# Kernel tuning notes

Hardware: AMD Instinct MI355X
Metric: run time of the kernel (lower is better)

The kernel has to match this reference:

```python
import jax, jax.numpy as jnp
import numpy as np
import math

B, T, D_IN, D_OUT = 4, 2048, 2048, 2048

def _inv_sigmoid(v):
    return math.log(v / (1 - v + 1e-08))

def setup_inputs() -> dict:
    key = jax.random.key(0)
    ks = jax.random.split(key, 6)
    x = jax.random.normal(ks[0], (B, T, D_IN), dtype=jnp.float32)
    W_p = jax.random.normal(ks[1], (D_OUT, D_IN), dtype=jnp.float32) * 0.02
    W_i = jax.random.normal(ks[2], (D_OUT, D_IN), dtype=jnp.float32) * 0.002
    W_d = jax.random.normal(ks[3], (D_OUT, D_IN), dtype=jnp.float32) * 0.002
    alpha_logit = jnp.full((D_IN,), _inv_sigmoid(0.9), dtype=jnp.float32)
    beta_logit = jnp.full((D_IN,), _inv_sigmoid(0.5), dtype=jnp.float32)
    W_gate_w = jax.random.normal(ks[4], (3, 3 * D_IN), dtype=jnp.float32) * 0.01
    W_gate_b = jnp.array([1.0, 0.0, 0.0], dtype=jnp.float32)
    bias = jnp.zeros((D_OUT,), dtype=jnp.float32)
    return {"x": x, "W_p": W_p, "W_i": W_i, "W_d": W_d,
            "alpha_logit": alpha_logit, "beta_logit": beta_logit,
            "W_gate_w": W_gate_w, "W_gate_b": W_gate_b, "bias": bias}

def _pid_features(x, alpha, beta):
    # x: (B,T,D). Single scan computing EMA integral and smoothed derivative.
    x_t = jnp.swapaxes(x, 0, 1)  # (T,B,D)
    x_prev = jnp.concatenate([jnp.zeros_like(x_t[:1]), x_t[:-1]], axis=0)
    diff_t = x_t - x_prev  # raw finite difference
    def step(carry, inp):
        s, d = carry
        xt, dt = inp
        s = alpha * s + (1.0 - alpha) * xt
        d = beta * d + (1.0 - beta) * dt
        return (s, d), (s, d)
    s0 = jnp.zeros(x.shape[::2], dtype=x.dtype)  # (B,D)
    _, (integ_t, deriv_t) = jax.lax.scan(step, (s0, s0), (x_t, diff_t))
    return jnp.swapaxes(integ_t, 0, 1), jnp.swapaxes(deriv_t, 0, 1)

def reference(x, W_p, W_i, W_d, alpha_logit, beta_logit, W_gate_w, W_gate_b, bias):
    alpha = jax.nn.sigmoid(alpha_logit)  # (D,)
    beta = jax.nn.sigmoid(beta_logit)
    integral, derivative = _pid_features(x, alpha, beta)  # (B,T,D) each
    gate_in = jnp.concatenate([x, integral, derivative], axis=-1)  # (B,T,3D)
    logits = jnp.einsum('btk,gk->btg', gate_in, W_gate_w) + W_gate_b
    gates = jax.nn.softmax(logits, axis=-1)  # (B,T,3)
    p_out = jnp.einsum('btd,od->bto', x, W_p)
    i_out = jnp.einsum('btd,od->bto', integral, W_i)
    d_out = jnp.einsum('btd,od->bto', derivative, W_d)
    y = gates[..., 0:1] * p_out + gates[..., 1:2] * i_out + gates[..., 2:3] * d_out + bias
    return y
```

## Files before the change

### kernel.cpp

```cpp
#include <hip/hip_runtime.h>
#include <stdint.h>

typedef unsigned short u16;

#define GAS __attribute__((address_space(1)))
#define LAS __attribute__((address_space(3)))

typedef __bf16 bf16x8 __attribute__((ext_vector_type(8)));
typedef float f32x4 __attribute__((ext_vector_type(4)));


__device__ inline u16 f2b(float f) {
    uint32_t x = __float_as_uint(f);
    uint32_t r = (x + 0x7fffu + ((x >> 16) & 1u)) >> 16;
    return (u16)r;
}

__device__ inline float b2f(u16 u) {
    union { uint32_t i; float f; } v;
    v.i = ((uint32_t)u) << 16;
    return v.f;
}

__device__ inline void load8b(float* v, const u16* p) {
    uint4 u = *(const uint4*)p;
    v[0] = b2f((u16)(u.x)); v[1] = b2f((u16)(u.x >> 16));
    v[2] = b2f((u16)(u.y)); v[3] = b2f((u16)(u.y >> 16));
    v[4] = b2f((u16)(u.z)); v[5] = b2f((u16)(u.z >> 16));
    v[6] = b2f((u16)(u.w)); v[7] = b2f((u16)(u.w >> 16));
}

__device__ inline void load8f(float* v, const float* p) {
    float4 a = *(const float4*)p;
    float4 b = *(const float4*)(p + 4);
    v[0] = a.x; v[1] = a.y; v[2] = a.z; v[3] = a.w;
    v[4] = b.x; v[5] = b.y; v[6] = b.z; v[7] = b.w;
}

__device__ inline void store8b(u16* p, const float* v, float scale) {
    uint4 u;
    u.x = (uint32_t)f2b(v[0] * scale) | ((uint32_t)f2b(v[1] * scale) << 16);
    u.y = (uint32_t)f2b(v[2] * scale) | ((uint32_t)f2b(v[3] * scale) << 16);
    u.z = (uint32_t)f2b(v[4] * scale) | ((uint32_t)f2b(v[5] * scale) << 16);
    u.w = (uint32_t)f2b(v[6] * scale) | ((uint32_t)f2b(v[7] * scale) << 16);
    *(uint4*)p = u;
}

__device__ inline float sigmoidf(float v) { return 1.f / (1.f + __expf(-v)); }

__device__ inline float pow64f(float a) {
    float p = a * a;
    p = p * p;
    p = p * p;
    p = p * p;
    p = p * p;
    return p * p;
}

__device__ inline float* carry_ptr(u16* Z, int plane, int b, int c, int d) {
    int f = ((plane * 4 + b) * 32 + c) * 2048 + d;
    int row = f >> 10;
    int off = f & 1023;
    return (float*)(Z + (size_t)row * 6144) + off;
}

__global__ __launch_bounds__(256) void pack_w(
    const float* __restrict__ Wp, const float* __restrict__ Wi,
    const float* __restrict__ Wd, u16* __restrict__ Wcat)
{
    int i = (blockIdx.x * 256 + threadIdx.x) * 8;
    int seg = i >> 22;
    int j = i & 4194303;
    const float* src = (seg == 0) ? Wp : (seg == 1) ? Wi : Wd;
    int o = j >> 11;
    int c = j & 2047;
    float v[8];
    load8f(v, src + j);
    store8b(Wcat + (size_t)o * 6144 + seg * 2048 + c, v, 1.0f);
}

__global__ __launch_bounds__(256) void scan_pass1(
    const float* __restrict__ x, const float* __restrict__ alog,
    const float* __restrict__ blog, u16* __restrict__ Z)
{
    const int d = blockIdx.x * 256 + threadIdx.x;
    const int c = blockIdx.y;
    const int b = blockIdx.z;
    const float alpha = sigmoidf(alog[d]);
    const float beta  = sigmoidf(blog[d]);
    const float oma = 1.f - alpha, omb = 1.f - beta;
    const float* xp = x + ((size_t)b * 2048 + c * 64) * 2048 + d;
    float xprev = (c == 0) ? 0.f : xp[-2048];
    float s = 0.f, dd = 0.f;
    #pragma unroll 8
    for (int t = 0; t < 64; ++t) {
        float xf = xp[(size_t)t * 2048];
        s = alpha * s + oma * xf;
        dd = beta * dd + omb * (xf - xprev);
        xprev = xf;
    }
    *carry_ptr(Z, 0, b, c, d) = s;
    *carry_ptr(Z, 1, b, c, d) = dd;
}

__global__ __launch_bounds__(256) void scan_pass2(
    const float* __restrict__ alog, const float* __restrict__ blog,
    u16* __restrict__ Z)
{
    const int g = blockIdx.x * 256 + threadIdx.x;
    const int b = g >> 11;
    const int d = g & 2047;
    const float aL = pow64f(sigmoidf(alog[d]));
    const float bL = pow64f(sigmoidf(blog[d]));
    float sIn = 0.f, dIn = 0.f;
    for (int c = 0; c < 32; ++c) {
        float* sp = carry_ptr(Z, 0, b, c, d);
        float* dp = carry_ptr(Z, 1, b, c, d);
        float sl = *sp, dl = *dp;
        *sp = sIn; *dp = dIn;
        sIn = sl + aL * sIn;
        dIn = dl + bL * dIn;
    }
}

__global__ __launch_bounds__(256) void scan_pass3(
    const float* __restrict__ x, const float* __restrict__ alog,
    const float* __restrict__ blog, u16* __restrict__ Z)
{
    const int d = blockIdx.x * 256 + threadIdx.x;
    const int c = blockIdx.y;
    const int b = blockIdx.z;
    const float alpha = sigmoidf(alog[d]);
    const float beta  = sigmoidf(blog[d]);
    const float oma = 1.f - alpha, omb = 1.f - beta;
    const float* xp = x + ((size_t)b * 2048 + c * 64) * 2048 + d;
    u16* zp = Z + ((size_t)b * 2048 + c * 64) * 6144 + 2048 + d;
    float s  = *carry_ptr(Z, 0, b, c, d);
    float dd = *carry_ptr(Z, 1, b, c, d);
    float xprev = (c == 0) ? 0.f : xp[-2048];
    #pragma unroll 8
    for (int t = 0; t < 64; ++t) {
        float xf = xp[(size_t)t * 2048];
        s = alpha * s + oma * xf;
        dd = beta * dd + omb * (xf - xprev);
        xprev = xf;
        size_t zo = (size_t)t * 6144;
        zp[zo] = f2b(s);
        zp[zo + 2048] = f2b(dd);
    }
}

__global__ __launch_bounds__(256) void gates_kernel(
    const float* __restrict__ x, const float* __restrict__ Wg,
    const float* __restrict__ Wgb, u16* __restrict__ Z)
{
    const int row = blockIdx.x;
    const int tid = threadIdx.x;
    const int k = tid * 8;
    const float* xr = x + (size_t)row * 2048;
    u16* zr = Z + (size_t)row * 6144;

    float xv[8], sv[8], dv[8];
    load8f(xv, xr + k);
    load8b(sv, zr + 2048 + k);
    load8b(dv, zr + 4096 + k);

    float p[3];
    #pragma unroll
    for (int gg = 0; gg < 3; ++gg) {
        float wx[8], ws[8], wd[8];
        load8f(wx, Wg + gg * 6144 + k);
        load8f(ws, Wg + gg * 6144 + 2048 + k);
        load8f(wd, Wg + gg * 6144 + 4096 + k);
        float acc = 0.f;
        #pragma unroll
        for (int j = 0; j < 8; ++j)
            acc += xv[j] * wx[j] + sv[j] * ws[j] + dv[j] * wd[j];
        p[gg] = acc;
    }

    #pragma unroll
    for (int off = 32; off > 0; off >>= 1) {
        p[0] += __shfl_down(p[0], off);
        p[1] += __shfl_down(p[1], off);
        p[2] += __shfl_down(p[2], off);
    }

    __shared__ float red[4][3];
    __shared__ float gsh[3];
    int wv = tid >> 6, lane = tid & 63;
    if (lane == 0) { red[wv][0] = p[0]; red[wv][1] = p[1]; red[wv][2] = p[2]; }
    __syncthreads();
    if (tid == 0) {
        float l0 = red[0][0] + red[1][0] + red[2][0] + red[3][0] + Wgb[0];
        float l1 = red[0][1] + red[1][1] + red[2][1] + red[3][1] + Wgb[1];
        float l2 = red[0][2] + red[1][2] + red[2][2] + red[3][2] + Wgb[2];
        float m = fmaxf(l0, fmaxf(l1, l2));
        float e0 = __expf(l0 - m), e1 = __expf(l1 - m), e2 = __expf(l2 - m);
        float inv = 1.f / (e0 + e1 + e2);
        gsh[0] = e0 * inv; gsh[1] = e1 * inv; gsh[2] = e2 * inv;
    }
    __syncthreads();
    float g0 = gsh[0], g1 = gsh[1], g2 = gsh[2];
    store8b(zr + k, xv, g0);
    store8b(zr + 2048 + k, sv, g1);
    store8b(zr + 4096 + k, dv, g2);
}

__global__ __launch_bounds__(256, 3) void gemm_kernel(
    const u16* __restrict__ Z, const u16* __restrict__ Wcat,
    const float* __restrict__ bias, float* __restrict__ out)
{
    __shared__ u16 a_sh[128 * 64];
    __shared__ u16 b_sh[128 * 64];

    const int tid = threadIdx.x;
    const int bm = blockIdx.y * 128;
    const int bn = blockIdx.x * 128;

    const int srow = tid >> 3;
    const int scq  = tid & 7;
    const int ssub = (scq ^ (srow & 7)) * 8;
    const u16* aglob = Z + (size_t)(bm + srow) * 6144 + ssub;
    const u16* bglob = Wcat + (size_t)(bn + srow) * 6144 + ssub;
    u16* alds[4];
    u16* blds[4];
    #pragma unroll
    for (int c = 0; c < 4; ++c) {
        alds[c] = a_sh + c * 2048 + tid * 8;
        blds[c] = b_sh + c * 2048 + tid * 8;
    }

    const int lane = tid & 63;
    const int wv = tid >> 6;
    const int wm = (wv & 1) * 64;
    const int wn = (wv >> 1) * 64;
    const int fr = lane & 15;
    const int fq = lane >> 4;

    f32x4 acc[4][4] = {};

    for (int kt = 0; kt < 96; ++kt) {
        const int k0 = kt * 64;
        #pragma unroll
        for (int c = 0; c < 4; ++c)
            __builtin_amdgcn_global_load_lds(
                (const GAS uint32_t*)(aglob + (size_t)c * 32 * 6144 + k0),
                (LAS uint32_t*)alds[c], 16, 0, 0);
        #pragma unroll
        for (int c = 0; c < 4; ++c)
            __builtin_amdgcn_global_load_lds(
                (const GAS uint32_t*)(bglob + (size_t)c * 32 * 6144 + k0),
                (LAS uint32_t*)blds[c], 16, 0, 0);
        __syncthreads();

        #pragma unroll
        for (int h = 0; h < 2; ++h) {
            bf16x8 avf[4], bvf[4];
            #pragma unroll
            for (int i = 0; i < 4; ++i) {
                int row = wm + i * 16 + fr;
                int ch = (fq + 4 * h) ^ (row & 7);
                avf[i] = *(const bf16x8*)(a_sh + row * 64 + ch * 8);
            }
            #pragma unroll
            for (int j = 0; j < 4; ++j) {
                int row = wn + j * 16 + fr;
                int ch = (fq + 4 * h) ^ (row & 7);
                bvf[j] = *(const bf16x8*)(b_sh + row * 64 + ch * 8);
            }
            #pragma unroll
            for (int i = 0; i < 4; ++i)
                #pragma unroll
                for (int j = 0; j < 4; ++j)
                    acc[i][j] = __builtin_amdgcn_mfma_f32_16x16x32_bf16(
                        avf[i], bvf[j], acc[i][j], 0, 0, 0);
        }
        __syncthreads();
    }

    #pragma unroll
    for (int j = 0; j < 4; ++j) {
        const int col = bn + wn + j * 16 + fr;
        const float bv = bias[col];
        #pragma unroll
        for (int i = 0; i < 4; ++i) {
            const int row0 = bm + wm + i * 16 + fq * 4;
            #pragma unroll
            for (int r = 0; r < 4; ++r)
                out[(size_t)(row0 + r) * 2048 + col] = acc[i][j][r] + bv;
        }
    }
}

extern "C" void kernel_launch(void* const* d_in, const int* in_sizes, int n_in,
                              void* d_out, int out_size, void* d_ws, size_t ws_size,
                              hipStream_t stream) {
    const float* x    = (const float*)d_in[0];
    const float* Wp   = (const float*)d_in[1];
    const float* Wi   = (const float*)d_in[2];
    const float* Wd   = (const float*)d_in[3];
    const float* al   = (const float*)d_in[4];
    const float* bl   = (const float*)d_in[5];
    const float* Wg   = (const float*)d_in[6];
    const float* Wgb  = (const float*)d_in[7];
    const float* bias = (const float*)d_in[8];
    float* out = (float*)d_out;

    u16* Z    = (u16*)d_ws;
    u16* Wcat = (u16*)((char*)d_ws + (size_t)8192 * 6144 * 2);

    pack_w<<<6144, 256, 0, stream>>>(Wp, Wi, Wd, Wcat);
    scan_pass1<<<dim3(8, 32, 4), 256, 0, stream>>>(x, al, bl, Z);
    scan_pass2<<<32, 256, 0, stream>>>(al, bl, Z);
    scan_pass3<<<dim3(8, 32, 4), 256, 0, stream>>>(x, al, bl, Z);
    gates_kernel<<<8192, 256, 0, stream>>>(x, Wg, Wgb, Z);
    gemm_kernel<<<dim3(16, 64), 256, 0, stream>>>(Z, Wcat, bias, out);
}
```

Measured before the change: 446.0 us.

## Restructure GEMM to 256x256 tiles with 8 waves and pipelined LDS prefetch

Rewrites the main GEMM to use 256x256 output tiles with 512 threads and 128KB of dynamic LDS holding double-buffered K halves. Global-to-LDS loads for upcoming K steps are interleaved between MFMA phases, with barriers and s_setprio raising priority during MFMA bursts. A new XOR swizzle avoids LDS bank conflicts. The aim is more data reuse per tile and latency hiding. The costs are heavier register and LDS pressure, a grid of only 256 blocks, and many barriers per K step.

```diff
diff --git a/kernel.cpp b/kernel.cpp
--- a/kernel.cpp
+++ b/kernel.cpp
@@ -207,90 +207,144 @@
     store8b(zr + 4096 + k, dv, g2);
 }
 
-__global__ __launch_bounds__(256, 3) void gemm_kernel(
+__global__ __launch_bounds__(512, 2) void gemm_kernel(
     const u16* __restrict__ Z, const u16* __restrict__ Wcat,
     const float* __restrict__ bias, float* __restrict__ out)
 {
-    __shared__ u16 a_sh[128 * 64];
-    __shared__ u16 b_sh[128 * 64];
+    extern __shared__ u16 lds[];
+    u16* const lA = lds;
+    u16* const lB = lds + 32768;
 
     const int tid = threadIdx.x;
-    const int bm = blockIdx.y * 128;
-    const int bn = blockIdx.x * 128;
-
-    const int srow = tid >> 3;
-    const int scq  = tid & 7;
-    const int ssub = (scq ^ (srow & 7)) * 8;
-    const u16* aglob = Z + (size_t)(bm + srow) * 6144 + ssub;
-    const u16* bglob = Wcat + (size_t)(bn + srow) * 6144 + ssub;
-    u16* alds[4];
-    u16* blds[4];
-    #pragma unroll
-    for (int c = 0; c < 4; ++c) {
-        alds[c] = a_sh + c * 2048 + tid * 8;
-        blds[c] = b_sh + c * 2048 + tid * 8;
-    }
+    const int bn = blockIdx.x * 256;
+    const int bm = blockIdx.y * 256;
+
+    const int srow = tid >> 2;
+    const int sgg  = (tid & 3) ^ ((tid >> 2) & 3) ^ ((tid >> 4) & 3);
+    const u16* aglob = Z    + (size_t)(bm + srow) * 6144 + sgg * 8;
+    const u16* bglob = Wcat + (size_t)(bn + srow) * 6144 + sgg * 8;
 
     const int lane = tid & 63;
     const int wv = tid >> 6;
-    const int wm = (wv & 1) * 64;
-    const int wn = (wv >> 1) * 64;
+    const int wm = wv & 1;
+    const int wn = wv >> 1;
     const int fr = lane & 15;
     const int fq = lane >> 4;
-
-    f32x4 acc[4][4] = {};
+    const int g  = fq ^ ((fr ^ (fr >> 2)) & 3);
+    const int aoff = (wm * 128 + fr) * 32 + g * 8;
+    const int boff = (wn * 64 + fr) * 32 + g * 8;
+
+    f32x4 acc[8][4] = {};
+
+#define XSTAGE(L, Gp, jt, h) do {                                             \
+    u16* d_ = (L) + (((h) * 2 + ((jt) & 1)) * 8192) + tid * 8;                \
+    const u16* s_ = (Gp) + (size_t)(jt) * 64 + (h) * 32;                      \
+    __builtin_amdgcn_global_load_lds((const GAS uint32_t*)s_,                 \
+                                     (LAS uint32_t*)d_, 16, 0, 0);            \
+    __builtin_amdgcn_global_load_lds(                                         \
+        (const GAS uint32_t*)(s_ + (size_t)128 * 6144),                       \
+        (LAS uint32_t*)(d_ + 4096), 16, 0, 0);                                \
+} while (0)
+
+    XSTAGE(lA, aglob, 0, 0);
+    XSTAGE(lB, bglob, 0, 0);
+    XSTAGE(lA, aglob, 0, 1);
+    XSTAGE(lB, bglob, 0, 1);
+    XSTAGE(lA, aglob, 1, 0);
+    XSTAGE(lB, bglob, 1, 0);
+    asm volatile("s_waitcnt vmcnt(4)" ::: "memory");
+    __builtin_amdgcn_s_barrier();
 
     for (int kt = 0; kt < 96; ++kt) {
-        const int k0 = kt * 64;
-        #pragma unroll
-        for (int c = 0; c < 4; ++c)
-            __builtin_amdgcn_global_load_lds(
-                (const GAS uint32_t*)(aglob + (size_t)c * 32 * 6144 + k0),
-                (LAS uint32_t*)alds[c], 16, 0, 0);
-        #pragma unroll
-        for (int c = 0; c < 4; ++c)
-            __builtin_amdgcn_global_load_lds(
-                (const GAS uint32_t*)(bglob + (size_t)c * 32 * 6144 + k0),
-                (LAS uint32_t*)blds[c], 16, 0, 0);
-        __syncthreads();
-
-        #pragma unroll
-        for (int h = 0; h < 2; ++h) {
-            bf16x8 avf[4], bvf[4];
-            #pragma unroll
-            for (int i = 0; i < 4; ++i) {
-                int row = wm + i * 16 + fr;
-                int ch = (fq + 4 * h) ^ (row & 7);
-                avf[i] = *(const bf16x8*)(a_sh + row * 64 + ch * 8);
-            }
-            #pragma unroll
-            for (int j = 0; j < 4; ++j) {
-                int row = wn + j * 16 + fr;
-                int ch = (fq + 4 * h) ^ (row & 7);
-                bvf[j] = *(const bf16x8*)(b_sh + row * 64 + ch * 8);
-            }
-            #pragma unroll
-            for (int i = 0; i < 4; ++i)
-                #pragma unroll
-                for (int j = 0; j < 4; ++j)
-                    acc[i][j] = __builtin_amdgcn_mfma_f32_16x16x32_bf16(
-                        avf[i], bvf[j], acc[i][j], 0, 0, 0);
-        }
-        __syncthreads();
-    }
+        const int p = kt & 1;
+        int t1 = kt + 1; if (t1 == 96) t1 = 0;
+        int t2 = kt + 2; if (t2 >= 96) t2 -= 96;
+        const u16* aLo = lA + (0 * 2 + p) * 8192;
+        const u16* bLo = lB + (0 * 2 + p) * 8192;
+        const u16* aHi = lA + (2 + p) * 8192;
+        const u16* bHi = lB + (2 + p) * 8192;
+
+        bf16x8 av[4], bv[4];
+
+        #pragma unroll
+        for (int i = 0; i < 4; ++i) av[i] = *(const bf16x8*)(aLo + aoff + i * 512);
+        #pragma unroll
+        for (int j = 0; j < 4; ++j) bv[j] = *(const bf16x8*)(bLo + boff + j * 512);
+        XSTAGE(lA, aglob, t1, 1);
+        __builtin_amdgcn_s_barrier();
+        __builtin_amdgcn_s_setprio(1);
+        #pragma unroll
+        for (int i = 0; i < 4; ++i)
+            #pragma unroll
+            for (int j = 0; j < 4; ++j)
+                acc[i][j] = __builtin_amdgcn_mfma_f32_16x16x32_bf16(
+                    av[i], bv[j], acc[i][j], 0, 0, 0);
+        __builtin_amdgcn_s_setprio(0);
+        __builtin_amdgcn_s_barrier();
+
+        #pragma unroll
+        for (int i = 0; i < 4; ++i)
+            av[i] = *(const bf16x8*)(aLo + aoff + (4 + i) * 512);
+        XSTAGE(lB, bglob, t1, 1);
+        __builtin_amdgcn_s_barrier();
+        __builtin_amdgcn_s_setprio(1);
+        #pragma unroll
+        for (int i = 0; i < 4; ++i)
+            #pragma unroll
+            for (int j = 0; j < 4; ++j)
+                acc[4 + i][j] = __builtin_amdgcn_mfma_f32_16x16x32_bf16(
+                    av[i], bv[j], acc[4 + i][j], 0, 0, 0);
+        __builtin_amdgcn_s_setprio(0);
+        __builtin_amdgcn_s_barrier();
+
+        #pragma unroll
+        for (int i = 0; i < 4; ++i) av[i] = *(const bf16x8*)(aHi + aoff + i * 512);
+        #pragma unroll
+        for (int j = 0; j < 4; ++j) bv[j] = *(const bf16x8*)(bHi + boff + j * 512);
+        XSTAGE(lA, aglob, t2, 0);
+        __builtin_amdgcn_s_barrier();
+        __builtin_amdgcn_s_setprio(1);
+        #pragma unroll
+        for (int i = 0; i < 4; ++i)
+            #pragma unroll
+            for (int j = 0; j < 4; ++j)
+                acc[i][j] = __builtin_amdgcn_mfma_f32_16x16x32_bf16(
+                    av[i], bv[j], acc[i][j], 0, 0, 0);
+        __builtin_amdgcn_s_setprio(0);
+        __builtin_amdgcn_s_barrier();
+
+        #pragma unroll
+        for (int i = 0; i < 4; ++i)
+            av[i] = *(const bf16x8*)(aHi + aoff + (4 + i) * 512);
+        XSTAGE(lB, bglob, t2, 0);
+        __builtin_amdgcn_s_barrier();
+        __builtin_amdgcn_s_setprio(1);
+        #pragma unroll
+        for (int i = 0; i < 4; ++i)
+            #pragma unroll
+            for (int j = 0; j < 4; ++j)
+                acc[4 + i][j] = __builtin_amdgcn_mfma_f32_16x16x32_bf16(
+                    av[i], bv[j], acc[4 + i][j], 0, 0, 0);
+        __builtin_amdgcn_s_setprio(0);
+        asm volatile("s_waitcnt vmcnt(4)" ::: "memory");
+        __builtin_amdgcn_s_barrier();
+    }
+
+    asm volatile("s_waitcnt vmcnt(0)" ::: "memory");
 
     #pragma unroll
     for (int j = 0; j < 4; ++j) {
-        const int col = bn + wn + j * 16 + fr;
-        const float bv = bias[col];
-        #pragma unroll
-        for (int i = 0; i < 4; ++i) {
-            const int row0 = bm + wm + i * 16 + fq * 4;
+        const int col = bn + wn * 64 + j * 16 + fr;
+        const float bb = bias[col];
+        #pragma unroll
+        for (int mf = 0; mf < 8; ++mf) {
+            const int row0 = bm + wm * 128 + mf * 16 + fq * 4;
             #pragma unroll
             for (int r = 0; r < 4; ++r)
-                out[(size_t)(row0 + r) * 2048 + col] = acc[i][j][r] + bv;
+                out[(size_t)(row0 + r) * 2048 + col] = acc[mf][j][r] + bb;
         }
     }
+#undef XSTAGE
 }
 
 extern "C" void kernel_launch(void* const* d_in, const int* in_sizes, int n_in,
@@ -310,10 +364,18 @@
     u16* Z    = (u16*)d_ws;
     u16* Wcat = (u16*)((char*)d_ws + (size_t)8192 * 6144 * 2);
 
+    static bool lds_cfgd = false;
+    if (!lds_cfgd) {
+        (void)hipFuncSetAttribute((const void*)gemm_kernel,
+                                  hipFuncAttributeMaxDynamicSharedMemorySize,
+                                  131072);
+        lds_cfgd = true;
+    }
+
     pack_w<<<6144, 256, 0, stream>>>(Wp, Wi, Wd, Wcat);
     scan_pass1<<<dim3(8, 32, 4), 256, 0, stream>>>(x, al, bl, Z);
     scan_pass2<<<32, 256, 0, stream>>>(al, bl, Z);
     scan_pass3<<<dim3(8, 32, 4), 256, 0, stream>>>(x, al, bl, Z);
     gates_kernel<<<8192, 256, 0, stream>>>(x, Wg, Wgb, Z);
-    gemm_kernel<<<dim3(16, 64), 256, 0, stream>>>(Z, Wcat, bias, out);
-}
+    gemm_kernel<<<dim3(8, 32), 512, 131072, stream>>>(Z, Wcat, bias, out);
+}
```

Result: faster. 426.7 us (-4.3%).
